# Kernel optimization log

Hardware: AMD Instinct MI355X
Metric: run time of the kernel (lower is better)

Reference implementation:

```python
import jax, jax.numpy as jnp
import numpy as np

# Winograd F(4x4, 3x3) transform matrices (wincnn convention, as in jiecaoyu/winograd)
BT = jnp.array([
    [4.,  0., -5.,  0., 1., 0.],
    [0., -4., -4.,  1., 1., 0.],
    [0.,  4., -4., -1., 1., 0.],
    [0., -2., -1.,  2., 1., 0.],
    [0.,  2., -1., -2., 1., 0.],
    [0.,  4.,  0., -5., 0., 1.]], dtype=jnp.float32)  # [6,6]
AT = jnp.array([
    [1., 1.,  1., 1.,  1., 0.],
    [0., 1., -1., 2., -2., 0.],
    [0., 1.,  1., 4.,  4., 0.],
    [0., 1., -1., 8., -8., 1.]], dtype=jnp.float32)  # [4,6]

KERNEL = 3
PAD = 1
GROUPS = 1
TILE_IN = 6   # input_tile_size
TILE_OUT = 4  # output_tile_size


def setup_inputs() -> dict:
    key = jax.random.key(0)
    k1, k2, k3 = jax.random.split(key, 3)
    N, Cin, H, W = 16, 64, 128, 128
    Cout = 64
    x = jax.random.normal(k1, (N, Cin, H, W), dtype=jnp.float32)
    # weight is stored in the Winograd (6x6 spectral) domain, as in the module
    weight = jax.random.normal(k2, (Cout, Cin // GROUPS, TILE_IN, TILE_IN), dtype=jnp.float32) * 0.01
    bias = jax.random.normal(k3, (Cout,), dtype=jnp.float32) * 0.01
    return {"x": x, "weight": weight, "bias": bias}


def reference(x, weight, bias):
    N, Cin, H0, W0 = x.shape
    Cout = weight.shape[0]
    g = GROUPS
    # conv padding
    x = jnp.pad(x, ((0, 0), (0, 0), (PAD, PAD), (PAD, PAD)))
    H = x.shape[2]
    out_w = H - KERNEL + 1
    # pad so output width is a multiple of the output tile size
    extra = (-out_w) % TILE_OUT
    if extra:
        x = jnp.pad(x, ((0, 0), (0, 0), (0, extra), (0, extra)))
    nt = (x.shape[2] - TILE_IN) // TILE_OUT + 1  # tiles per spatial dim
    # extract overlapping 6x6 tiles with stride 4 (the torch unfold)
    idx = jnp.arange(nt)[:, None] * TILE_OUT + jnp.arange(TILE_IN)[None, :]  # [nt,6]
    tiles = x[:, :, idx]                 # [N,C,nt,6,Wp]
    tiles = tiles[:, :, :, :, idx]       # [N,C,nt,6,nt,6]
    # input transform: V = BT @ d @ BT^T per tile -> [N,C,nt,nt,6,6]
    V = jnp.einsum('ai,ncpiqj,bj->ncpqab', BT, tiles, BT)
    # grouped spectral GEMM over input channels
    Vg = V.reshape(N, g, Cin // g, nt, nt, TILE_IN, TILE_IN)
    Wg = weight.reshape(g, Cout // g, Cin // g, TILE_IN, TILE_IN)
    M = jnp.einsum('goiab,ngipqab->ngopqab', Wg, Vg)
    M = M.reshape(N, Cout, nt, nt, TILE_IN, TILE_IN)
    # output transform: Y = AT @ M @ AT^T per tile -> [N,O,nt,nt,4,4]
    Y = jnp.einsum('xa,nopqab,yb->nopqxy', AT, M, AT)
    # stitch tiles back: [N,O,nt,4,nt,4] -> [N,O,nt*4,nt*4]
    y = Y.transpose(0, 1, 2, 4, 3, 5).reshape(N, Cout, nt * TILE_OUT, nt * TILE_OUT)
    y = y + bias[None, :, None, None]
    # crop the extra padding
    y = y[:, :, :out_w, :out_w]
    return y
```

## Files before the change

kernel.cpp:

```cpp
#include <hip/hip_runtime.h>
#include <stdint.h>

typedef __attribute__((ext_vector_type(4))) float f32x4;
typedef __attribute__((ext_vector_type(8))) short s16x8;

#define WB_BYTES 294912

__device__ __forceinline__ short f2bf(float f) {
    uint32_t u = __builtin_bit_cast(uint32_t, f);
    u = u + 0x7FFFu + ((u >> 16) & 1u);
    return (short)(u >> 16);
}

__global__ __launch_bounds__(256) void wtrans(const float* __restrict__ wf, short* __restrict__ wb) {
    int tid = blockIdx.x * 256 + threadIdx.x;
    const float* src = wf + tid * 36;
    float w[36];
#pragma unroll
    for (int i = 0; i < 9; i++) {
        f32x4 v = *(const f32x4*)(src + 4 * i);
        w[4*i+0] = v[0]; w[4*i+1] = v[1]; w[4*i+2] = v[2]; w[4*i+3] = v[3];
    }
#pragma unroll
    for (int ab = 0; ab < 36; ab++) wb[ab * 4096 + tid] = f2bf(w[ab]);
}

#define XS 343
__global__ __launch_bounds__(256, 2) void wino_fused(const float* __restrict__ x,
                                                     const short* __restrict__ wb,
                                                     const float* __restrict__ bias,
                                                     float* __restrict__ out) {
    __shared__ float X[32 * XS];
    __shared__ __align__(16) short Vs[18 * 16 * 32];
    int t = threadIdx.x;
    int lane = t & 63;
    int cog = t >> 6;
    int lo = lane & 15;
    int kq = lane >> 4;

    int b = blockIdx.x;
    int n = b >> 6;
    int sb = b & 63;
    int p0 = (sb >> 3) * 4;
    int q0 = (sb & 7) * 4;
    const float* xb = x + (size_t)n * 64 * 16384;
    int row0 = 4 * p0 - 1;
    int col0a = 4 * q0 - 4;

    int cin = t & 31;
    int tl0 = t >> 5;

    f32x4 acc[36];
#pragma unroll
    for (int i = 0; i < 36; i++) acc[i] = (f32x4){0.f, 0.f, 0.f, 0.f};

#pragma unroll
    for (int r = 0; r < 2; r++) {
#pragma unroll
        for (int i = 0; i < 14; i++) {
            int s = i * 256 + t;
            if (s < 3456) {
                int ci = s / 108;
                int rs = s - ci * 108;
                int row = rs / 6;
                int c4 = rs - row * 6;
                int gr = row0 + row;
                int gc = col0a + 4 * c4;
                float v0 = 0.f, v1 = 0.f, v2 = 0.f, v3 = 0.f;
                if ((unsigned)gr < 128u) {
                    const float* rowp = xb + (size_t)((r * 32 + ci) * 128 + gr) * 128;
                    if (gc >= 0 && gc + 3 < 128) {
                        f32x4 v = *(const f32x4*)(rowp + gc);
                        v0 = v[0]; v1 = v[1]; v2 = v[2]; v3 = v[3];
                    } else {
                        if ((unsigned)(gc + 0) < 128u) v0 = rowp[gc + 0];
                        if ((unsigned)(gc + 1) < 128u) v1 = rowp[gc + 1];
                        if ((unsigned)(gc + 2) < 128u) v2 = rowp[gc + 2];
                        if ((unsigned)(gc + 3) < 128u) v3 = rowp[gc + 3];
                    }
                }
                int base = ci * XS + row * 18;
                int cl = 4 * c4 - 3;
                if ((unsigned)(cl + 0) < 18u) X[base + cl + 0] = v0;
                if ((unsigned)(cl + 1) < 18u) X[base + cl + 1] = v1;
                if ((unsigned)(cl + 2) < 18u) X[base + cl + 2] = v2;
                if ((unsigned)(cl + 3) < 18u) X[base + cl + 3] = v3;
            }
        }
        __syncthreads();

#pragma unroll
        for (int s = 0; s < 2; s++) {
#pragma unroll
            for (int task = 0; task < 2; task++) {
                int tl = tl0 + task * 8;
                int tp = tl >> 2, tq = tl & 3;
                const float* Xb = X + cin * XS + (4 * tp) * 18 + 4 * tq;
                float Ua[3][6];
#pragma unroll
                for (int c = 0; c < 6; c++) {
                    float m0 = Xb[0 * 18 + c], m1 = Xb[1 * 18 + c], m2 = Xb[2 * 18 + c];
                    float m3 = Xb[3 * 18 + c], m4 = Xb[4 * 18 + c], m5 = Xb[5 * 18 + c];
                    if (s == 0) {
                        float e = fmaf(-4.f, m2, m4);
                        float f = fmaf(-4.f, m1, m3);
                        Ua[0][c] = fmaf(4.f, m0 - m2, m4 - m2);
                        Ua[1][c] = e + f;
                        Ua[2][c] = e - f;
                    } else {
                        float g = m4 - m2;
                        float h = m3 - m1;
                        Ua[0][c] = fmaf(2.f, h, g);
                        Ua[1][c] = fmaf(-2.f, h, g);
                        Ua[2][c] = fmaf(4.f, m1 - m3, m5 - m3);
                    }
                }
                short* vb = Vs + tl * 32 + cin;
#pragma unroll
                for (int ar = 0; ar < 3; ar++) {
                    float m0 = Ua[ar][0], m1 = Ua[ar][1], m2 = Ua[ar][2];
                    float m3 = Ua[ar][3], m4 = Ua[ar][4], m5 = Ua[ar][5];
                    float e = fmaf(-4.f, m2, m4);
                    float f = fmaf(-4.f, m1, m3);
                    float g = m4 - m2;
                    float h = m3 - m1;
                    vb[(ar * 6 + 0) * 512] = f2bf(fmaf(4.f, m0 - m2, g));
                    vb[(ar * 6 + 1) * 512] = f2bf(e + f);
                    vb[(ar * 6 + 2) * 512] = f2bf(e - f);
                    vb[(ar * 6 + 3) * 512] = f2bf(fmaf(2.f, h, g));
                    vb[(ar * 6 + 4) * 512] = f2bf(fmaf(-2.f, h, g));
                    vb[(ar * 6 + 5) * 512] = f2bf(fmaf(4.f, m1 - m3, m5 - m3));
                }
            }
            __syncthreads();

            const short* wb_base = wb + (s * 18) * 4096 + (cog * 16 + lo) * 64 + r * 32 + kq * 8;
            const short* v_base = Vs + lo * 32 + kq * 8;
#pragma unroll
            for (int abl = 0; abl < 18; abl++) {
                s16x8 a0 = *(const s16x8*)(wb_base + abl * 4096);
                s16x8 b0 = *(const s16x8*)(v_base + abl * 512);
                acc[s * 18 + abl] = __builtin_amdgcn_mfma_f32_16x16x32_bf16(a0, b0, acc[s * 18 + abl], 0, 0, 0);
            }
            __syncthreads();
        }
    }

    int p = p0 + (lo >> 2);
    int q = q0 + (lo & 3);
#pragma unroll
    for (int rr = 0; rr < 4; rr++) {
        int co = cog * 16 + kq * 4 + rr;
        float bv = bias[co];
        float z[4][6];
#pragma unroll
        for (int bb = 0; bb < 6; bb++) {
            float m0 = acc[0 * 6 + bb][rr], m1 = acc[1 * 6 + bb][rr], m2 = acc[2 * 6 + bb][rr];
            float m3 = acc[3 * 6 + bb][rr], m4 = acc[4 * 6 + bb][rr], m5 = acc[5 * 6 + bb][rr];
            float s1 = m1 + m2, d1 = m1 - m2, s2 = m3 + m4, d2 = m3 - m4;
            z[0][bb] = m0 + s1 + s2;
            z[1][bb] = fmaf(2.f, d2, d1);
            z[2][bb] = fmaf(4.f, s2, s1);
            z[3][bb] = fmaf(8.f, d2, d1) + m5;
        }
        float* ob = out + ((size_t)(n * 64 + co) * 128 + 4 * p) * 128 + 4 * q;
#pragma unroll
        for (int xr = 0; xr < 4; xr++) {
            float s1 = z[xr][1] + z[xr][2], d1 = z[xr][1] - z[xr][2];
            float s2 = z[xr][3] + z[xr][4], d2 = z[xr][3] - z[xr][4];
            f32x4 y;
            y[0] = z[xr][0] + s1 + s2 + bv;
            y[1] = fmaf(2.f, d2, d1) + bv;
            y[2] = fmaf(4.f, s2, s1) + bv;
            y[3] = fmaf(8.f, d2, d1) + z[xr][5] + bv;
            *(f32x4*)(ob + xr * 128) = y;
        }
    }
}

extern "C" void kernel_launch(void* const* d_in, const int* in_sizes, int n_in,
                              void* d_out, int out_size, void* d_ws, size_t ws_size,
                              hipStream_t stream) {
    const float* x    = (const float*)d_in[0];
    const float* wf   = (const float*)d_in[1];
    const float* bias = (const float*)d_in[2];
    float* out = (float*)d_out;

    if (ws_size < WB_BYTES) return;
    short* wb = (short*)d_ws;

    wtrans<<<16, 256, 0, stream>>>(wf, wb);
    wino_fused<<<1024, 256, 0, stream>>>(x, wb, bias, out);
}
```

Measured before the change: 181.8 us.

## Split Cout across blocks, halve per-thread accumulators, switch to fp16 MFMA

The fused Winograd kernel now splits output channels in two across blocks, doubling the grid. Within a block, the 36 spectral positions are split between wave pairs, which cuts per-thread accumulators from 36 to 18 and lets launch bounds request 4 blocks per SIMD. Partial output transforms are combined through shared memory, and block IDs are remapped to interleave work. Operands change from bf16 16x16x32 MFMA to fp16 16x16x16 MFMA with Cin staged in 16-channel chunks. The cost is that each block redoes the input transform for its half of the channels, and fp16 range and precision differ from bf16.

After: 290.6 us. +59.8%, slower.

```diff
diff --git a/kernel.cpp b/kernel.cpp
--- a/kernel.cpp
+++ b/kernel.cpp
@@ -2,17 +2,11 @@
 #include <stdint.h>
 
 typedef __attribute__((ext_vector_type(4))) float f32x4;
-typedef __attribute__((ext_vector_type(8))) short s16x8;
+typedef __attribute__((ext_vector_type(4))) _Float16 f16x4;
 
 #define WB_BYTES 294912
 
-__device__ __forceinline__ short f2bf(float f) {
-    uint32_t u = __builtin_bit_cast(uint32_t, f);
-    u = u + 0x7FFFu + ((u >> 16) & 1u);
-    return (short)(u >> 16);
-}
-
-__global__ __launch_bounds__(256) void wtrans(const float* __restrict__ wf, short* __restrict__ wb) {
+__global__ __launch_bounds__(256) void wtrans(const float* __restrict__ wf, _Float16* __restrict__ wh) {
     int tid = blockIdx.x * 256 + threadIdx.x;
     const float* src = wf + tid * 36;
     float w[36];
@@ -22,53 +16,61 @@
         w[4*i+0] = v[0]; w[4*i+1] = v[1]; w[4*i+2] = v[2]; w[4*i+3] = v[3];
     }
 #pragma unroll
-    for (int ab = 0; ab < 36; ab++) wb[ab * 4096 + tid] = f2bf(w[ab]);
+    for (int ab = 0; ab < 36; ab++) wh[ab * 4096 + tid] = (_Float16)w[ab];
 }
 
 #define XS 343
-__global__ __launch_bounds__(256, 2) void wino_fused(const float* __restrict__ x,
-                                                     const short* __restrict__ wb,
+__global__ __launch_bounds__(256, 4) void wino_fused(const float* __restrict__ x,
+                                                     const _Float16* __restrict__ wh,
                                                      const float* __restrict__ bias,
                                                      float* __restrict__ out) {
-    __shared__ float X[32 * XS];
-    __shared__ __align__(16) short Vs[18 * 16 * 32];
+    __shared__ __align__(16) float SM[10096];
+    float* X = SM;
+    _Float16* Vs = (_Float16*)(SM + 16 * XS);
+    float* P = SM;
+
     int t = threadIdx.x;
     int lane = t & 63;
-    int cog = t >> 6;
+    int w = t >> 6;
+    int sh = w >> 1;
+    int cog = w & 1;
     int lo = lane & 15;
     int kq = lane >> 4;
 
     int b = blockIdx.x;
-    int n = b >> 6;
-    int sb = b & 63;
+    int vid = (b & 7) * 256 + (b >> 3);
+    int ch = vid & 1;
+    int sb = (vid >> 1) & 63;
+    int n = vid >> 7;
+
     int p0 = (sb >> 3) * 4;
     int q0 = (sb & 7) * 4;
     const float* xb = x + (size_t)n * 64 * 16384;
     int row0 = 4 * p0 - 1;
     int col0a = 4 * q0 - 4;
 
-    int cin = t & 31;
-    int tl0 = t >> 5;
-
-    f32x4 acc[36];
-#pragma unroll
-    for (int i = 0; i < 36; i++) acc[i] = (f32x4){0.f, 0.f, 0.f, 0.f};
-
-#pragma unroll
-    for (int r = 0; r < 2; r++) {
-#pragma unroll
-        for (int i = 0; i < 14; i++) {
+    int tl = t >> 4;
+    int ci = t & 15;
+    int tp = tl >> 2, tq = tl & 3;
+
+    f32x4 acc[18];
+#pragma unroll
+    for (int i = 0; i < 18; i++) acc[i] = (f32x4){0.f, 0.f, 0.f, 0.f};
+
+    for (int rq = 0; rq < 4; ++rq) {
+#pragma unroll
+        for (int i = 0; i < 7; i++) {
             int s = i * 256 + t;
-            if (s < 3456) {
-                int ci = s / 108;
-                int rs = s - ci * 108;
+            if (s < 1728) {
+                int cis = s / 108;
+                int rs = s - cis * 108;
                 int row = rs / 6;
                 int c4 = rs - row * 6;
                 int gr = row0 + row;
                 int gc = col0a + 4 * c4;
                 float v0 = 0.f, v1 = 0.f, v2 = 0.f, v3 = 0.f;
                 if ((unsigned)gr < 128u) {
-                    const float* rowp = xb + (size_t)((r * 32 + ci) * 128 + gr) * 128;
+                    const float* rowp = xb + (size_t)((rq * 16 + cis) * 128 + gr) * 128;
                     if (gc >= 0 && gc + 3 < 128) {
                         f32x4 v = *(const f32x4*)(rowp + gc);
                         v0 = v[0]; v1 = v[1]; v2 = v[2]; v3 = v[3];
@@ -79,7 +81,7 @@
                         if ((unsigned)(gc + 3) < 128u) v3 = rowp[gc + 3];
                     }
                 }
-                int base = ci * XS + row * 18;
+                int base = cis * XS + row * 18;
                 int cl = 4 * c4 - 3;
                 if ((unsigned)(cl + 0) < 18u) X[base + cl + 0] = v0;
                 if ((unsigned)(cl + 1) < 18u) X[base + cl + 1] = v1;
@@ -89,33 +91,29 @@
         }
         __syncthreads();
 
-#pragma unroll
-        for (int s = 0; s < 2; s++) {
-#pragma unroll
-            for (int task = 0; task < 2; task++) {
-                int tl = tl0 + task * 8;
-                int tp = tl >> 2, tq = tl & 3;
-                const float* Xb = X + cin * XS + (4 * tp) * 18 + 4 * tq;
+        {
+            const float* Xb = X + ci * XS + (4 * tp) * 18 + 4 * tq;
+            _Float16* vb = Vs + tl * 16 + ci;
+#pragma unroll
+            for (int s2 = 0; s2 < 2; s2++) {
                 float Ua[3][6];
 #pragma unroll
                 for (int c = 0; c < 6; c++) {
                     float m0 = Xb[0 * 18 + c], m1 = Xb[1 * 18 + c], m2 = Xb[2 * 18 + c];
                     float m3 = Xb[3 * 18 + c], m4 = Xb[4 * 18 + c], m5 = Xb[5 * 18 + c];
-                    if (s == 0) {
+                    if (s2 == 0) {
                         float e = fmaf(-4.f, m2, m4);
                         float f = fmaf(-4.f, m1, m3);
                         Ua[0][c] = fmaf(4.f, m0 - m2, m4 - m2);
                         Ua[1][c] = e + f;
                         Ua[2][c] = e - f;
                     } else {
-                        float g = m4 - m2;
-                        float h = m3 - m1;
+                        float g = m4 - m2, h = m3 - m1;
                         Ua[0][c] = fmaf(2.f, h, g);
                         Ua[1][c] = fmaf(-2.f, h, g);
                         Ua[2][c] = fmaf(4.f, m1 - m3, m5 - m3);
                     }
                 }
-                short* vb = Vs + tl * 32 + cin;
 #pragma unroll
                 for (int ar = 0; ar < 3; ar++) {
                     float m0 = Ua[ar][0], m1 = Ua[ar][1], m2 = Ua[ar][2];
@@ -124,56 +122,89 @@
                     float f = fmaf(-4.f, m1, m3);
                     float g = m4 - m2;
                     float h = m3 - m1;
-                    vb[(ar * 6 + 0) * 512] = f2bf(fmaf(4.f, m0 - m2, g));
-                    vb[(ar * 6 + 1) * 512] = f2bf(e + f);
-                    vb[(ar * 6 + 2) * 512] = f2bf(e - f);
-                    vb[(ar * 6 + 3) * 512] = f2bf(fmaf(2.f, h, g));
-                    vb[(ar * 6 + 4) * 512] = f2bf(fmaf(-2.f, h, g));
-                    vb[(ar * 6 + 5) * 512] = f2bf(fmaf(4.f, m1 - m3, m5 - m3));
+                    int abb = (s2 * 3 + ar) * 6;
+                    vb[(abb + 0) * 256] = (_Float16)fmaf(4.f, m0 - m2, g);
+                    vb[(abb + 1) * 256] = (_Float16)(e + f);
+                    vb[(abb + 2) * 256] = (_Float16)(e - f);
+                    vb[(abb + 3) * 256] = (_Float16)fmaf(2.f, h, g);
+                    vb[(abb + 4) * 256] = (_Float16)fmaf(-2.f, h, g);
+                    vb[(abb + 5) * 256] = (_Float16)fmaf(4.f, m1 - m3, m5 - m3);
                 }
             }
-            __syncthreads();
-
-            const short* wb_base = wb + (s * 18) * 4096 + (cog * 16 + lo) * 64 + r * 32 + kq * 8;
-            const short* v_base = Vs + lo * 32 + kq * 8;
+        }
+        __syncthreads();
+
+        {
+            const _Float16* wbh = wh + (sh * 18) * 4096 + (size_t)(ch * 32 + cog * 16 + lo) * 64 + rq * 16 + kq * 4;
+            const _Float16* vb2 = Vs + (sh * 18) * 256 + lo * 16 + kq * 4;
 #pragma unroll
             for (int abl = 0; abl < 18; abl++) {
-                s16x8 a0 = *(const s16x8*)(wb_base + abl * 4096);
-                s16x8 b0 = *(const s16x8*)(v_base + abl * 512);
-                acc[s * 18 + abl] = __builtin_amdgcn_mfma_f32_16x16x32_bf16(a0, b0, acc[s * 18 + abl], 0, 0, 0);
-            }
-            __syncthreads();
-        }
-    }
-
+                f16x4 a = *(const f16x4*)(wbh + abl * 4096);
+                f16x4 bf = *(const f16x4*)(vb2 + abl * 256);
+                acc[abl] = __builtin_amdgcn_mfma_f32_16x16x16f16(a, bf, acc[abl], 0, 0, 0);
+            }
+        }
+    }
+
+    __syncthreads();
     int p = p0 + (lo >> 2);
     int q = q0 + (lo & 3);
-#pragma unroll
-    for (int rr = 0; rr < 4; rr++) {
-        int co = cog * 16 + kq * 4 + rr;
-        float bv = bias[co];
-        float z[4][6];
-#pragma unroll
-        for (int bb = 0; bb < 6; bb++) {
-            float m0 = acc[0 * 6 + bb][rr], m1 = acc[1 * 6 + bb][rr], m2 = acc[2 * 6 + bb][rr];
-            float m3 = acc[3 * 6 + bb][rr], m4 = acc[4 * 6 + bb][rr], m5 = acc[5 * 6 + bb][rr];
-            float s1 = m1 + m2, d1 = m1 - m2, s2 = m3 + m4, d2 = m3 - m4;
-            z[0][bb] = m0 + s1 + s2;
-            z[1][bb] = fmaf(2.f, d2, d1);
-            z[2][bb] = fmaf(4.f, s2, s1);
-            z[3][bb] = fmaf(8.f, d2, d1) + m5;
-        }
-        float* ob = out + ((size_t)(n * 64 + co) * 128 + 4 * p) * 128 + 4 * q;
-#pragma unroll
-        for (int xr = 0; xr < 4; xr++) {
-            float s1 = z[xr][1] + z[xr][2], d1 = z[xr][1] - z[xr][2];
-            float s2 = z[xr][3] + z[xr][4], d2 = z[xr][3] - z[xr][4];
-            f32x4 y;
-            y[0] = z[xr][0] + s1 + s2 + bv;
-            y[1] = fmaf(2.f, d2, d1) + bv;
-            y[2] = fmaf(4.f, s2, s1) + bv;
-            y[3] = fmaf(8.f, d2, d1) + z[xr][5] + bv;
-            *(f32x4*)(ob + xr * 128) = y;
+
+    if (sh == 1) {
+#pragma unroll
+        for (int rr = 0; rr < 4; rr++) {
+            float z[4][6];
+#pragma unroll
+            for (int bb = 0; bb < 6; bb++) {
+                float m3 = acc[bb][rr], m4 = acc[6 + bb][rr], m5 = acc[12 + bb][rr];
+                float sv = m3 + m4, dv = m3 - m4;
+                z[0][bb] = sv;
+                z[1][bb] = 2.f * dv;
+                z[2][bb] = 4.f * sv;
+                z[3][bb] = fmaf(8.f, dv, m5);
+            }
+#pragma unroll
+            for (int xr = 0; xr < 4; xr++) {
+                float s1 = z[xr][1] + z[xr][2], d1 = z[xr][1] - z[xr][2];
+                float s2 = z[xr][3] + z[xr][4], d2 = z[xr][3] - z[xr][4];
+                f32x4 y;
+                y[0] = z[xr][0] + s1 + s2;
+                y[1] = fmaf(2.f, d2, d1);
+                y[2] = fmaf(4.f, s2, s1);
+                y[3] = fmaf(8.f, d2, d1) + z[xr][5];
+                *(f32x4*)&P[cog * 4096 + (rr * 4 + xr) * 256 + lane * 4] = y;
+            }
+        }
+    }
+    __syncthreads();
+    if (sh == 0) {
+#pragma unroll
+        for (int rr = 0; rr < 4; rr++) {
+            int co = ch * 32 + cog * 16 + kq * 4 + rr;
+            float bv = bias[co];
+            float z[4][6];
+#pragma unroll
+            for (int bb = 0; bb < 6; bb++) {
+                float m0 = acc[bb][rr], m1 = acc[6 + bb][rr], m2 = acc[12 + bb][rr];
+                float s1 = m1 + m2, d1 = m1 - m2;
+                z[0][bb] = m0 + s1;
+                z[1][bb] = d1;
+                z[2][bb] = s1;
+                z[3][bb] = d1;
+            }
+            float* ob = out + ((size_t)(n * 64 + co) * 128 + 4 * p) * 128 + 4 * q;
+#pragma unroll
+            for (int xr = 0; xr < 4; xr++) {
+                float s1 = z[xr][1] + z[xr][2], d1 = z[xr][1] - z[xr][2];
+                float s2 = z[xr][3] + z[xr][4], d2 = z[xr][3] - z[xr][4];
+                f32x4 part = *(const f32x4*)&P[cog * 4096 + (rr * 4 + xr) * 256 + lane * 4];
+                f32x4 y;
+                y[0] = z[xr][0] + s1 + s2 + part[0] + bv;
+                y[1] = fmaf(2.f, d2, d1) + part[1] + bv;
+                y[2] = fmaf(4.f, s2, s1) + part[2] + bv;
+                y[3] = fmaf(8.f, d2, d1) + z[xr][5] + part[3] + bv;
+                *(f32x4*)(ob + xr * 128) = y;
+            }
         }
     }
 }
@@ -187,8 +218,8 @@
     float* out = (float*)d_out;
 
     if (ws_size < WB_BYTES) return;
-    short* wb = (short*)d_ws;
-
-    wtrans<<<16, 256, 0, stream>>>(wf, wb);
-    wino_fused<<<1024, 256, 0, stream>>>(x, wb, bias, out);
+    _Float16* wh = (_Float16*)d_ws;
+
+    wtrans<<<16, 256, 0, stream>>>(wf, wh);
+    wino_fused<<<2048, 256, 0, stream>>>(x, wh, bias, out);
 }
```
